# Kernel tuning notes

Measured on AMD Instinct MI355X. Metric: run time of the kernel, lower is better.

## Reference

```python
import jax, jax.numpy as jnp
import numpy as np

N = 100000
IN_CH = 512
HEADS = 8
OUT_CH = 1  # forced: nn.Linear(heads, 1) consumes GAT output of size heads*out_channels
E = 3200000
NEG_SLOPE = 0.2


def setup_inputs() -> dict:
    key = jax.random.key(0)
    ks = jax.random.split(key, 8)
    x = jax.random.normal(ks[0], (N, IN_CH), dtype=jnp.float32)
    edge_index = jax.random.randint(ks[1], (2, E), 0, N, dtype=jnp.int32)
    # GATConv params
    W = jax.random.normal(ks[2], (IN_CH, HEADS * OUT_CH), dtype=jnp.float32) / np.sqrt(IN_CH)
    att_src = jax.random.normal(ks[3], (HEADS, OUT_CH), dtype=jnp.float32)
    att_dst = jax.random.normal(ks[4], (HEADS, OUT_CH), dtype=jnp.float32)
    gat_bias = jnp.zeros((HEADS * OUT_CH,), dtype=jnp.float32)
    # calibration head
    lin_w = jax.random.normal(ks[5], (1, HEADS), dtype=jnp.float32) / np.sqrt(HEADS)
    lin_b = jnp.zeros((1,), dtype=jnp.float32)
    bias = jnp.ones((1,), dtype=jnp.float32)  # init bias value 1.0
    return {"x": x, "edge_index": edge_index, "W": W, "att_src": att_src,
            "att_dst": att_dst, "gat_bias": gat_bias, "lin_w": lin_w,
            "lin_b": lin_b, "bias": bias}


def reference(x, edge_index, W, att_src, att_dst, gat_bias, lin_w, lin_b, bias):
    n = x.shape[0]
    # GATConv adds self-loops by default
    loops = jnp.arange(n, dtype=edge_index.dtype)
    src = jnp.concatenate([edge_index[0], loops])
    dst = jnp.concatenate([edge_index[1], loops])

    h = (x @ W).reshape(n, HEADS, OUT_CH)                 # [N,H,C]
    a_src = (h * att_src[None]).sum(-1)                   # [N,H]
    a_dst = (h * att_dst[None]).sum(-1)                   # [N,H]

    e = jax.nn.leaky_relu(a_src[src] + a_dst[dst], NEG_SLOPE)  # [Etot,H]
    # segment softmax over incoming edges of each dst node
    e_max = jax.ops.segment_max(e, dst, num_segments=n)        # [N,H]
    e_exp = jnp.exp(e - e_max[dst])
    denom = jax.ops.segment_sum(e_exp, dst, num_segments=n)
    alpha = e_exp / (denom[dst] + 1e-16)                       # [Etot,H]

    msg = h[src] * alpha[..., None]                            # [Etot,H,C]
    out = jax.ops.segment_sum(msg, dst, num_segments=n)        # [N,H,C]
    out = out.reshape(n, HEADS * OUT_CH) + gat_bias            # concat heads

    temperature = jax.nn.relu(out @ lin_w.T + lin_b) + bias    # [N,1]
    return temperature
```

## Files before the change

kernel.cpp:

```cpp
#include <hip/hip_runtime.h>

#define IN_CH 512
#define HEADS 8
#define NEG_SLOPE 0.2f

#define RB 256
#define RB_BITS 8
#define NB_MAX 400
#define LCAP 8
#define BCAP 9216
#define GT_STRIDE 16
#define EPT 9

__device__ __forceinline__ float lrelu(float v) {
    return v > 0.f ? v : NEG_SLOPE * v;
}

__device__ __forceinline__ void gemm_rows(const float* __restrict__ x,
                                          const float* __restrict__ W,
                                          float* __restrict__ h, int n,
                                          int wave, int nwav, int lane) {
    float4 wlo[8], whi[8];
#pragma unroll
    for (int j = 0; j < 8; ++j) {
        int k = (j < 4) ? (lane * 4 + j) : (256 + lane * 4 + (j - 4));
        const float4* p = (const float4*)(W + k * 8);
        wlo[j] = p[0];
        whi[j] = p[1];
    }
    for (int row = wave; row < n; row += nwav) {
        const float4* xr = (const float4*)(x + (size_t)row * IN_CH);
        float4 x0 = xr[lane];
        float4 x1 = xr[64 + lane];
        float xs[8] = {x0.x, x0.y, x0.z, x0.w, x1.x, x1.y, x1.z, x1.w};
        float acc[8] = {0.f, 0.f, 0.f, 0.f, 0.f, 0.f, 0.f, 0.f};
#pragma unroll
        for (int j = 0; j < 8; ++j) {
            acc[0] = fmaf(xs[j], wlo[j].x, acc[0]);
            acc[1] = fmaf(xs[j], wlo[j].y, acc[1]);
            acc[2] = fmaf(xs[j], wlo[j].z, acc[2]);
            acc[3] = fmaf(xs[j], wlo[j].w, acc[3]);
            acc[4] = fmaf(xs[j], whi[j].x, acc[4]);
            acc[5] = fmaf(xs[j], whi[j].y, acc[5]);
            acc[6] = fmaf(xs[j], whi[j].z, acc[6]);
            acc[7] = fmaf(xs[j], whi[j].w, acc[7]);
        }
#pragma unroll
        for (int off = 32; off >= 1; off >>= 1) {
#pragma unroll
            for (int hd = 0; hd < 8; ++hd)
                acc[hd] += __shfl_down(acc[hd], off, 64);
        }
        if (lane == 0) {
            float4* hp = (float4*)(h + (size_t)row * 8);
            hp[0] = make_float4(acc[0], acc[1], acc[2], acc[3]);
            hp[1] = make_float4(acc[4], acc[5], acc[6], acc[7]);
        }
    }
}

__global__ __launch_bounds__(256, 4)
void k_fused(const float* __restrict__ x, const float* __restrict__ W,
             float* __restrict__ h, const int* __restrict__ ei,
             int* __restrict__ gtail, int* __restrict__ bucket,
             int n, int E, int gemmBlocks, int nb) {
    __shared__ int lcnt[NB_MAX];
    __shared__ int gbase[NB_MAX];
    __shared__ int lst[NB_MAX * LCAP];

    if ((int)blockIdx.x < gemmBlocks) {
        const int lane = threadIdx.x & 63;
        const int wave = (int)((blockIdx.x * 256 + threadIdx.x) >> 6);
        gemm_rows(x, W, h, n, wave, gemmBlocks * 4, lane);
        return;
    }

    for (int i = threadIdx.x; i < nb; i += 256) lcnt[i] = 0;
    __syncthreads();

    int sb = blockIdx.x - gemmBlocks;
    int base = sb * 2048 + (int)threadIdx.x * 8;
    if (base < E) {
        if (base + 8 <= E) {
            int4 s0 = *(const int4*)(ei + base);
            int4 s1 = *(const int4*)(ei + base + 4);
            int4 d0 = *(const int4*)(ei + E + base);
            int4 d1 = *(const int4*)(ei + E + base + 4);
            int ss[8] = {s0.x, s0.y, s0.z, s0.w, s1.x, s1.y, s1.z, s1.w};
            int dd[8] = {d0.x, d0.y, d0.z, d0.w, d1.x, d1.y, d1.z, d1.w};
#pragma unroll
            for (int k = 0; k < 8; ++k) {
                int b = dd[k] >> RB_BITS;
                int v = (ss[k] << RB_BITS) | (dd[k] & (RB - 1));
                int p = atomicAdd(&lcnt[b], 1);
                if (p < LCAP) {
                    lst[b * LCAP + p] = v;
                } else {
                    int g = atomicAdd(gtail + (b << 4), 1);
                    if (g < BCAP) bucket[(size_t)b * BCAP + g] = v;
                }
            }
        } else {
            for (int k = 0; base + k < E; ++k) {
                int s = ei[base + k];
                int d = ei[E + base + k];
                int b = d >> RB_BITS;
                int v = (s << RB_BITS) | (d & (RB - 1));
                int p = atomicAdd(&lcnt[b], 1);
                if (p < LCAP) {
                    lst[b * LCAP + p] = v;
                } else {
                    int g = atomicAdd(gtail + (b << 4), 1);
                    if (g < BCAP) bucket[(size_t)b * BCAP + g] = v;
                }
            }
        }
    }
    __syncthreads();

    for (int b = threadIdx.x; b < nb; b += 256) {
        int c = min(lcnt[b], LCAP);
        gbase[b] = c ? atomicAdd(gtail + (b << 4), c) : 0;
    }
    __syncthreads();

    int tot = nb * LCAP;
    for (int pr = threadIdx.x; pr < tot; pr += 256) {
        int b = pr >> 3;
        int i = pr & (LCAP - 1);
        if (i < min(lcnt[b], LCAP)) {
            int pos = gbase[b] + i;
            if (pos < BCAP) bucket[(size_t)b * BCAP + pos] = lst[b * LCAP + i];
        }
    }
}

__global__ __launch_bounds__(1024, 4)
void k_agg(const float* __restrict__ h, const int* __restrict__ bucket,
           const int* __restrict__ gtail,
           const float* __restrict__ att_src, const float* __restrict__ att_dst,
           const float* __restrict__ gat_bias, const float* __restrict__ lin_w,
           const float* __restrict__ lin_b, const float* __restrict__ bias,
           float* __restrict__ out, int n) {
    __shared__ int elds[BCAP];
    __shared__ float hw[HEADS][RB];
    __shared__ int cnt[RB];
    __shared__ int scn[RB];
    __shared__ int pcnt[RB];

    const int b = blockIdx.x;
    const int base = b << RB_BITS;
    const int Wn = min(RB, n - base);
    const int tid = threadIdx.x;

    for (int i = tid; i < RB; i += 1024) { cnt[i] = 0; pcnt[i] = 0; }
    for (int i = tid; i < Wn * 8; i += 1024)
        hw[i & 7][i >> 3] = h[(size_t)(base + (i >> 3)) * 8 + (i & 7)];

    const int tail = min(gtail[b << 4], BCAP);
    const int* __restrict__ lstp = bucket + (size_t)b * BCAP;

    int vv[EPT];
#pragma unroll
    for (int r = 0; r < EPT; ++r) {
        int idx = tid + r * 1024;
        vv[r] = (idx < tail) ? lstp[idx] : -1;
    }
    __syncthreads();
#pragma unroll
    for (int r = 0; r < EPT; ++r)
        if (vv[r] >= 0) atomicAdd(&cnt[vv[r] & (RB - 1)], 1);
    __syncthreads();

    if (tid < RB) scn[tid] = cnt[tid];
    __syncthreads();
    for (int off = 1; off < RB; off <<= 1) {
        int v = 0;
        if (tid < RB) {
            v = scn[tid];
            if (tid >= off) v += scn[tid - off];
        }
        __syncthreads();
        if (tid < RB) scn[tid] = v;
        __syncthreads();
    }

#pragma unroll
    for (int r = 0; r < EPT; ++r) {
        if (vv[r] >= 0) {
            int ln = vv[r] & (RB - 1);
            int pos = scn[ln] - cnt[ln] + atomicAdd(&pcnt[ln], 1);
            if (pos < BCAP) elds[pos] = vv[r] >> RB_BITS;
        }
    }
    __syncthreads();

    float as[8], ad[8];
#pragma unroll
    for (int q = 0; q < 8; ++q) { as[q] = att_src[q]; ad[q] = att_dst[q]; }

    const int ln = tid >> 2;
    const int j = tid & 3;
    float num[8] = {0.f, 0.f, 0.f, 0.f, 0.f, 0.f, 0.f, 0.f};
    float den[8] = {0.f, 0.f, 0.f, 0.f, 0.f, 0.f, 0.f, 0.f};
    if (ln < Wn) {
        float hadd[8];
#pragma unroll
        for (int q = 0; q < 8; ++q) hadd[q] = hw[q][ln] * ad[q];
        const int deg = cnt[ln];
        const int st = scn[ln] - deg;
        int i = j;
        for (; i + 4 < deg; i += 8) {
            int s0 = elds[st + i];
            int s1 = elds[st + i + 4];
            const float4* p0 = (const float4*)(h + (size_t)s0 * 8);
            const float4* p1 = (const float4*)(h + (size_t)s1 * 8);
            float4 a0 = p0[0], b0 = p0[1];
            float4 a1 = p1[0], b1 = p1[1];
            float h0[8] = {a0.x, a0.y, a0.z, a0.w, b0.x, b0.y, b0.z, b0.w};
            float h1[8] = {a1.x, a1.y, a1.z, a1.w, b1.x, b1.y, b1.z, b1.w};
#pragma unroll
            for (int q = 0; q < 8; ++q) {
                float e0 = lrelu(fmaf(h0[q], as[q], hadd[q]));
                float p0e = __expf(e0);
                den[q] += p0e;
                num[q] = fmaf(p0e, h0[q], num[q]);
                float e1 = lrelu(fmaf(h1[q], as[q], hadd[q]));
                float p1e = __expf(e1);
                den[q] += p1e;
                num[q] = fmaf(p1e, h1[q], num[q]);
            }
        }
        for (; i < deg; i += 4) {
            int s = elds[st + i];
            const float4* hp = (const float4*)(h + (size_t)s * 8);
            float4 ha = hp[0], hb = hp[1];
            float hs[8] = {ha.x, ha.y, ha.z, ha.w, hb.x, hb.y, hb.z, hb.w};
#pragma unroll
            for (int q = 0; q < 8; ++q) {
                float e = lrelu(fmaf(hs[q], as[q], hadd[q]));
                float p = __expf(e);
                den[q] += p;
                num[q] = fmaf(p, hs[q], num[q]);
            }
        }
    }
#pragma unroll
    for (int q = 0; q < 8; ++q) {
        num[q] += __shfl_xor(num[q], 1, 64);
        num[q] += __shfl_xor(num[q], 2, 64);
        den[q] += __shfl_xor(den[q], 1, 64);
        den[q] += __shfl_xor(den[q], 2, 64);
    }

    if (ln < Wn && j == 0) {
        float t = 0.f;
        float lb = lin_b[0], bs = bias[0];
#pragma unroll
        for (int q = 0; q < 8; ++q) {
            float hv = hw[q][ln];
            float e = lrelu(hv * (as[q] + ad[q]));
            float p = __expf(e);
            float nm = fmaf(p, hv, num[q]);
            float dn = den[q] + p;
            float o = nm / (dn + 1e-16f) + gat_bias[q];
            t = fmaf(o, lin_w[q], t);
        }
        out[base + ln] = fmaxf(t + lb, 0.f) + bs;
    }
}

extern "C" void kernel_launch(void* const* d_in, const int* in_sizes, int n_in,
                              void* d_out, int out_size, void* d_ws, size_t ws_size,
                              hipStream_t stream) {
    const float* x = (const float*)d_in[0];
    const int* ei = (const int*)d_in[1];
    const float* W = (const float*)d_in[2];
    const float* att_src = (const float*)d_in[3];
    const float* att_dst = (const float*)d_in[4];
    const float* gat_bias = (const float*)d_in[5];
    const float* lin_w = (const float*)d_in[6];
    const float* lin_b = (const float*)d_in[7];
    const float* bias = (const float*)d_in[8];

    const int n = in_sizes[0] / IN_CH;
    const int E = in_sizes[1] / 2;
    const int nb = (n + RB - 1) >> RB_BITS;

    float* h = (float*)d_ws;
    int* gtail = (int*)(h + (size_t)n * HEADS);
    int* bucket = gtail + (size_t)nb * GT_STRIDE;

    hipMemsetAsync(gtail, 0, (size_t)nb * GT_STRIDE * sizeof(int), stream);

    const int GB = 1024;
    const int SB = (E + 2047) / 2048;
    k_fused<<<GB + SB, 256, 0, stream>>>(x, W, h, ei, gtail, bucket, n, E, GB, nb);
    k_agg<<<nb, 1024, 0, stream>>>(h, bucket, gtail, att_src, att_dst,
                                   gat_bias, lin_w, lin_b, bias,
                                   (float*)d_out, n);
}
```

Before: 364.5 us.

## Shrink dst buckets, restructure GEMV lane mapping, deepen gather unroll in aggregation

The x@W GEMV is remapped so that each lane holds 64 weights for one head and one K-slice and processes two rows per iteration, with a shuffle-xor reduction replacing the 6-step reduction over all 8 heads. Destination buckets shrink from 256 to 128 nodes, and the aggregation kernel moves to 512-thread blocks with twice as many blocks, to raise parallelism and cut LDS per block. The edge gather loop is unrolled to 4 independent h loads per iteration for more memory-level parallelism. In exchange, the GEMV holds 64 weight registers per lane, and with BCAP 4800 a bucket that exceeds its capacity drops edges.

```diff
diff --git a/kernel.cpp b/kernel.cpp
--- a/kernel.cpp
+++ b/kernel.cpp
@@ -4,13 +4,13 @@
 #define HEADS 8
 #define NEG_SLOPE 0.2f
 
-#define RB 256
-#define RB_BITS 8
-#define NB_MAX 400
+#define RB 128
+#define RB_BITS 7
+#define NB_MAX 784
 #define LCAP 8
-#define BCAP 9216
+#define BCAP 4800
 #define GT_STRIDE 16
-#define EPT 9
+#define EPT 10
 
 __device__ __forceinline__ float lrelu(float v) {
     return v > 0.f ? v : NEG_SLOPE * v;
@@ -20,46 +20,63 @@
                                           const float* __restrict__ W,
                                           float* __restrict__ h, int n,
                                           int wave, int nwav, int lane) {
-    float4 wlo[8], whi[8];
-#pragma unroll
-    for (int j = 0; j < 8; ++j) {
-        int k = (j < 4) ? (lane * 4 + j) : (256 + lane * 4 + (j - 4));
-        const float4* p = (const float4*)(W + k * 8);
-        wlo[j] = p[0];
-        whi[j] = p[1];
-    }
-    for (int row = wave; row < n; row += nwav) {
-        const float4* xr = (const float4*)(x + (size_t)row * IN_CH);
-        float4 x0 = xr[lane];
-        float4 x1 = xr[64 + lane];
-        float xs[8] = {x0.x, x0.y, x0.z, x0.w, x1.x, x1.y, x1.z, x1.w};
-        float acc[8] = {0.f, 0.f, 0.f, 0.f, 0.f, 0.f, 0.f, 0.f};
-#pragma unroll
-        for (int j = 0; j < 8; ++j) {
-            acc[0] = fmaf(xs[j], wlo[j].x, acc[0]);
-            acc[1] = fmaf(xs[j], wlo[j].y, acc[1]);
-            acc[2] = fmaf(xs[j], wlo[j].z, acc[2]);
-            acc[3] = fmaf(xs[j], wlo[j].w, acc[3]);
-            acc[4] = fmaf(xs[j], whi[j].x, acc[4]);
-            acc[5] = fmaf(xs[j], whi[j].y, acc[5]);
-            acc[6] = fmaf(xs[j], whi[j].z, acc[6]);
-            acc[7] = fmaf(xs[j], whi[j].w, acc[7]);
-        }
-#pragma unroll
-        for (int off = 32; off >= 1; off >>= 1) {
-#pragma unroll
-            for (int hd = 0; hd < 8; ++hd)
-                acc[hd] += __shfl_down(acc[hd], off, 64);
-        }
-        if (lane == 0) {
-            float4* hp = (float4*)(h + (size_t)row * 8);
-            hp[0] = make_float4(acc[0], acc[1], acc[2], acc[3]);
-            hp[1] = make_float4(acc[4], acc[5], acc[6], acc[7]);
-        }
-    }
-}
-
-__global__ __launch_bounds__(256, 4)
+    const int hq = lane & 7;
+    const int kb = lane >> 3;
+    float wf[64];
+#pragma unroll
+    for (int i = 0; i < 64; ++i)
+        wf[i] = W[(kb * 64 + i) * 8 + hq];
+
+    const int npairs = n >> 1;
+    for (int pr = wave; pr < npairs; pr += nwav) {
+        const int rA = pr * 2;
+        const float4* xa = (const float4*)(x + (size_t)rA * IN_CH) + kb * 16;
+        const float4* xb = (const float4*)(x + (size_t)(rA + 1) * IN_CH) + kb * 16;
+        float accA = 0.f, accB = 0.f;
+#pragma unroll
+        for (int c = 0; c < 16; ++c) {
+            float4 va = xa[c];
+            float4 vb = xb[c];
+            accA = fmaf(va.x, wf[c * 4 + 0], accA);
+            accA = fmaf(va.y, wf[c * 4 + 1], accA);
+            accA = fmaf(va.z, wf[c * 4 + 2], accA);
+            accA = fmaf(va.w, wf[c * 4 + 3], accA);
+            accB = fmaf(vb.x, wf[c * 4 + 0], accB);
+            accB = fmaf(vb.y, wf[c * 4 + 1], accB);
+            accB = fmaf(vb.z, wf[c * 4 + 2], accB);
+            accB = fmaf(vb.w, wf[c * 4 + 3], accB);
+        }
+        accA += __shfl_xor(accA, 8, 64);
+        accA += __shfl_xor(accA, 16, 64);
+        accA += __shfl_xor(accA, 32, 64);
+        accB += __shfl_xor(accB, 8, 64);
+        accB += __shfl_xor(accB, 16, 64);
+        accB += __shfl_xor(accB, 32, 64);
+        if (lane < 16) {
+            float v = (lane < 8) ? accA : accB;
+            h[(size_t)rA * 8 + lane] = v;
+        }
+    }
+    if ((n & 1) && wave == 0) {
+        const int r = n - 1;
+        const float4* xr = (const float4*)(x + (size_t)r * IN_CH) + kb * 16;
+        float acc = 0.f;
+#pragma unroll
+        for (int c = 0; c < 16; ++c) {
+            float4 v = xr[c];
+            acc = fmaf(v.x, wf[c * 4 + 0], acc);
+            acc = fmaf(v.y, wf[c * 4 + 1], acc);
+            acc = fmaf(v.z, wf[c * 4 + 2], acc);
+            acc = fmaf(v.w, wf[c * 4 + 3], acc);
+        }
+        acc += __shfl_xor(acc, 8, 64);
+        acc += __shfl_xor(acc, 16, 64);
+        acc += __shfl_xor(acc, 32, 64);
+        if (lane < 8) h[(size_t)r * 8 + hq] = acc;
+    }
+}
+
+__global__ __launch_bounds__(256)
 void k_fused(const float* __restrict__ x, const float* __restrict__ W,
              float* __restrict__ h, const int* __restrict__ ei,
              int* __restrict__ gtail, int* __restrict__ bucket,
@@ -135,7 +152,7 @@
     }
 }
 
-__global__ __launch_bounds__(1024, 4)
+__global__ __launch_bounds__(512)
 void k_agg(const float* __restrict__ h, const int* __restrict__ bucket,
            const int* __restrict__ gtail,
            const float* __restrict__ att_src, const float* __restrict__ att_dst,
@@ -153,8 +170,8 @@
     const int Wn = min(RB, n - base);
     const int tid = threadIdx.x;
 
-    for (int i = tid; i < RB; i += 1024) { cnt[i] = 0; pcnt[i] = 0; }
-    for (int i = tid; i < Wn * 8; i += 1024)
+    if (tid < RB) { cnt[tid] = 0; pcnt[tid] = 0; }
+    for (int i = tid; i < Wn * 8; i += 512)
         hw[i & 7][i >> 3] = h[(size_t)(base + (i >> 3)) * 8 + (i & 7)];
 
     const int tail = min(gtail[b << 4], BCAP);
@@ -163,7 +180,7 @@
     int vv[EPT];
 #pragma unroll
     for (int r = 0; r < EPT; ++r) {
-        int idx = tid + r * 1024;
+        int idx = tid + r * 512;
         vv[r] = (idx < tail) ? lstp[idx] : -1;
     }
     __syncthreads();
@@ -210,25 +227,27 @@
         const int deg = cnt[ln];
         const int st = scn[ln] - deg;
         int i = j;
-        for (; i + 4 < deg; i += 8) {
-            int s0 = elds[st + i];
-            int s1 = elds[st + i + 4];
-            const float4* p0 = (const float4*)(h + (size_t)s0 * 8);
-            const float4* p1 = (const float4*)(h + (size_t)s1 * 8);
-            float4 a0 = p0[0], b0 = p0[1];
-            float4 a1 = p1[0], b1 = p1[1];
-            float h0[8] = {a0.x, a0.y, a0.z, a0.w, b0.x, b0.y, b0.z, b0.w};
-            float h1[8] = {a1.x, a1.y, a1.z, a1.w, b1.x, b1.y, b1.z, b1.w};
-#pragma unroll
-            for (int q = 0; q < 8; ++q) {
-                float e0 = lrelu(fmaf(h0[q], as[q], hadd[q]));
-                float p0e = __expf(e0);
-                den[q] += p0e;
-                num[q] = fmaf(p0e, h0[q], num[q]);
-                float e1 = lrelu(fmaf(h1[q], as[q], hadd[q]));
-                float p1e = __expf(e1);
-                den[q] += p1e;
-                num[q] = fmaf(p1e, h1[q], num[q]);
+        for (; i + 12 < deg; i += 16) {
+            int sv[4] = {elds[st + i], elds[st + i + 4],
+                         elds[st + i + 8], elds[st + i + 12]};
+            float4 pa[4], pb[4];
+#pragma unroll
+            for (int k = 0; k < 4; ++k) {
+                const float4* hp = (const float4*)(h + (size_t)sv[k] * 8);
+                pa[k] = hp[0];
+                pb[k] = hp[1];
+            }
+#pragma unroll
+            for (int k = 0; k < 4; ++k) {
+                float hs[8] = {pa[k].x, pa[k].y, pa[k].z, pa[k].w,
+                               pb[k].x, pb[k].y, pb[k].z, pb[k].w};
+#pragma unroll
+                for (int q = 0; q < 8; ++q) {
+                    float e = lrelu(fmaf(hs[q], as[q], hadd[q]));
+                    float p = __expf(e);
+                    den[q] += p;
+                    num[q] = fmaf(p, hs[q], num[q]);
+                }
             }
         }
         for (; i < deg; i += 4) {
@@ -296,7 +315,7 @@
     const int GB = 1024;
     const int SB = (E + 2047) / 2048;
     k_fused<<<GB + SB, 256, 0, stream>>>(x, W, h, ei, gtail, bucket, n, E, GB, nb);
-    k_agg<<<nb, 1024, 0, stream>>>(h, bucket, gtail, att_src, att_dst,
-                                   gat_bias, lin_w, lin_b, bias,
-                                   (float*)d_out, n);
-}
+    k_agg<<<nb, 512, 0, stream>>>(h, bucket, gtail, att_src, att_dst,
+                                  gat_bias, lin_w, lin_b, bias,
+                                  (float*)d_out, n);
+}
```

Result: slower. 409.6 us (+12.4%).
